# Optimization experiments

Measured on AMD Instinct MI355X. Metric: run time of the kernel, lower is better.

The kernel has to match this reference:

```python
import jax, jax.numpy as jnp
import numpy as np

TINY = 1e-15
EPS = 1e-6  # float32 eps from the torch module
C = 1.0
S = 1.0 / np.sqrt(C)
SQRTC = np.sqrt(C)


def _sinhc(z):
    # stable sinh(z)/z with small-argument Taylor branch
    y = jnp.sinh(z) / jnp.maximum(z, EPS)
    y0 = 1.0 + z * z / 6.0
    return jnp.where(jnp.abs(z) < EPS, y0, y)


def _beta(x):
    denom = jnp.sqrt(1.0 + C * jnp.sum(x * x, axis=-1, keepdims=True))
    return 1.0 / jnp.maximum(denom, TINY)


def _log0(y):
    s = jnp.linalg.norm(y, axis=-1, keepdims=True)
    coef = jnp.arcsinh(s / S) / jnp.maximum(s / S, EPS)
    return coef * y


def _exp0(v):
    r = jnp.linalg.norm(v, axis=-1, keepdims=True)
    coef = jnp.sinh(r / S) / jnp.maximum(r / S, EPS)
    return coef * v


def _proj_tan0(v, max_norm=20.0):
    r = jnp.maximum(jnp.linalg.norm(v, axis=-1, keepdims=True), EPS)
    return jnp.minimum(max_norm / r, 1.0) * v


def _pt_0_to_y(y, v):
    b = _beta(y)
    coef = C * b / (1.0 + b)
    dot = jnp.sum(y * v, axis=-1, keepdims=True)
    return v + coef * dot * y


def _gyro_add(x, y):
    b_x = _beta(x)
    b_y = _beta(y)
    s2 = S * S
    xy = jnp.sum(x * y, axis=-1, keepdims=True)
    coef = b_x / (1.0 + b_x) * (xy / s2) + (1.0 - b_y) / b_y
    return x + y + coef * x


def _exp_map(x, v):
    s2 = S * S
    x_norm2 = jnp.sum(x * x, axis=-1, keepdims=True)
    v_norm2 = jnp.sum(v * v, axis=-1, keepdims=True)
    dot_x_v = jnp.sum(x * v, axis=-1, keepdims=True)
    g_pvv = jnp.maximum(v_norm2 - dot_x_v * dot_x_v / (s2 + x_norm2), TINY)
    r_g = jnp.sqrt(g_pvv)
    b_x = _beta(x)
    coef1 = b_x / (1.0 + b_x)
    coef2 = -(C * b_x ** 3) / jnp.maximum(1.0 + b_x, TINY) ** 2
    dpi_v = coef1 * v + coef2 * dot_x_v * x
    lambda_x = (1.0 + b_x) / jnp.maximum(b_x, TINY)
    z_arg = jnp.clip(SQRTC * r_g, -20.0, 20.0)
    w = lambda_x * _sinhc(z_arg) * dpi_v
    return _gyro_add(x, w)


def setup_inputs() -> dict:
    key = jax.random.key(0)
    k1, k2, k3 = jax.random.split(key, 3)
    N, D_IN, D_OUT = 16384, 2048, 2048
    x = jax.random.normal(k1, (N, D_IN), dtype=jnp.float32)
    # weight scaled ~1/sqrt(d_in) so tangent norms stay in a sane hyperbolic range
    W = jax.random.normal(k2, (D_OUT, D_IN), dtype=jnp.float32) * (1.0 / np.sqrt(D_IN))
    b = jax.random.normal(k3, (D_OUT,), dtype=jnp.float32) * 0.01
    return {"x": x, "W": W, "b": b}


def reference(x, W, b):
    # PV fully-connected layer: log map -> linear -> exp map -> transported bias
    v = _log0(x)                 # [N, d_in] tangent at origin
    u = v @ W.T                  # [N, d_out]
    u = _proj_tan0(u)            # tangent norm clamp (max_norm=20)
    y = _exp0(u)                 # [N, d_out] PV point
    bt = _pt_0_to_y(y, b)        # parallel transport bias tangent 0 -> y
    out = _exp_map(y, bt)        # geodesic step (includes gyro_add)
    return out
```

## Files before the change

### kernel.cpp

```cpp
#include <hip/hip_runtime.h>
#include <stdint.h>

typedef __bf16 bf16_t;
typedef __bf16 bf16x8 __attribute__((ext_vector_type(8)));
typedef float floatx4 __attribute__((ext_vector_type(4)));
typedef float f32x4 __attribute__((ext_vector_type(4)));

#define N_ROWS 16384
#define D_IN   2048
#define D_OUT  2048
#define EPSF   1e-6f
#define TINYF  1e-15f

#define BM 256
#define BN 256
#define BK 32
#define NT 192

__device__ __forceinline__ void load_lds16(const void* g, void* l) {
    __builtin_amdgcn_global_load_lds(
        (const __attribute__((address_space(1))) unsigned int*)(const unsigned int*)g,
        (__attribute__((address_space(3))) unsigned int*)(unsigned int*)l,
        16, 0, 0);
}

__global__ __launch_bounds__(256) void pvfc_wsplit(
    const float* __restrict__ W, bf16_t* __restrict__ Wh, bf16_t* __restrict__ Wl)
{
    const size_t i = ((size_t)blockIdx.x * 256 + threadIdx.x) * 8;
    f32x4 a = *(const f32x4*)(W + i);
    f32x4 c = *(const f32x4*)(W + i + 4);
    float v[8] = {a.x, a.y, a.z, a.w, c.x, c.y, c.z, c.w};
    bf16x8 hv, lv;
#pragma unroll
    for (int j = 0; j < 8; ++j) {
        const bf16_t h = (bf16_t)v[j];
        hv[j] = h;
        lv[j] = (bf16_t)(v[j] - (float)h);
    }
    *(bf16x8*)(Wh + i) = hv;
    *(bf16x8*)(Wl + i) = lv;
}

__global__ __launch_bounds__(256) void pvfc_prologue(
    const float* __restrict__ x, bf16_t* __restrict__ Ap)
{
    __shared__ float red[4];
    const int row = blockIdx.x, tid = threadIdx.x;
    const int lane = tid & 63, wave = tid >> 6;

    const float* xr = x + (size_t)row * D_IN + tid * 8;
    f32x4 a = __builtin_nontemporal_load((const f32x4*)xr);
    f32x4 c = __builtin_nontemporal_load((const f32x4*)(xr + 4));
    float v[8] = {a.x, a.y, a.z, a.w, c.x, c.y, c.z, c.w};

    float s = 0.f;
#pragma unroll
    for (int i = 0; i < 8; ++i) s += v[i] * v[i];
#pragma unroll
    for (int off = 32; off > 0; off >>= 1) s += __shfl_down(s, off, 64);
    if (lane == 0) red[wave] = s;
    __syncthreads();
    const float s2  = red[0] + red[1] + red[2] + red[3];
    const float nrm = sqrtf(s2);
    const float coef = asinhf(nrm) / fmaxf(nrm, EPSF);

    bf16x8 hv, lv;
#pragma unroll
    for (int j = 0; j < 8; ++j) {
        const float vi = coef * v[j];
        const bf16_t h = (bf16_t)vi;
        hv[j] = h;
        lv[j] = (bf16_t)(vi - (float)h);
    }
    bf16_t* ar = Ap + (size_t)row * (2 * D_IN);
    *(bf16x8*)(ar + tid * 8)         = hv;
    *(bf16x8*)(ar + D_IN + tid * 8)  = lv;
}

#define BAR __builtin_amdgcn_s_barrier()
#define SCHED_FENCE __builtin_amdgcn_sched_barrier(0)
#define WAIT_LGKM0 do { asm volatile("s_waitcnt lgkmcnt(0)" ::: "memory"); \
                        __builtin_amdgcn_sched_barrier(0); } while (0)
#define WAIT_VM0   do { asm volatile("s_waitcnt vmcnt(0)" ::: "memory");   \
                        __builtin_amdgcn_sched_barrier(0); } while (0)

#define READ_A4(AF, brd, h)                                                    \
    _Pragma("unroll")                                                          \
    for (int i = 0; i < 4; ++i) {                                              \
        const int mi = (h) * 4 + i;                                            \
        AF[mi] = *(const bf16x8*)&As3[(brd) * 8192 +                           \
                    (wm * 128 + mi * 16 + m16) * 32 + ((quad ^ swk) * 8)];     \
    }
#define READ_B4(BF, brd)                                                       \
    _Pragma("unroll")                                                          \
    for (int j = 0; j < 4; ++j)                                                \
        BF[j] = *(const bf16x8*)&Bs3[(brd) * 8192 +                            \
                    (wn * 64 + j * 16 + m16) * 32 + ((quad ^ swk) * 8)];
#define MFMA_G(AF, BF, g)                                                      \
    do {                                                                       \
        __builtin_amdgcn_s_setprio(1);                                         \
        _Pragma("unroll")                                                      \
        for (int i = 0; i < 2; ++i)                                            \
            _Pragma("unroll")                                                  \
            for (int j = 0; j < 4; ++j)                                        \
                acc[(g) * 2 + i][j] = __builtin_amdgcn_mfma_f32_16x16x32_bf16( \
                    AF[(g) * 2 + i], BF[j], acc[(g) * 2 + i][j], 0, 0, 0);     \
        __builtin_amdgcn_s_setprio(0);                                         \
    } while (0)

#define BODY(AC, BC, AN, BN_, brd, bst, stT)                                   \
    do {                                                                       \
        WAIT_LGKM0;                 \
        stage_tile(stT, bst);                 \
        SCHED_FENCE;                                                           \
        READ_A4(AN, brd, 0); MFMA_G(AC, BC, 0); SCHED_FENCE;                   \
        READ_A4(AN, brd, 1); MFMA_G(AC, BC, 1); SCHED_FENCE;                   \
        READ_B4(BN_, brd);   MFMA_G(AC, BC, 2); SCHED_FENCE;                   \
        MFMA_G(AC, BC, 3);                                                     \
        WAIT_VM0;                                                              \
        BAR;                                                                   \
    } while (0)

__global__ __launch_bounds__(512, 2) void pvfc_gemm(
    const bf16_t* __restrict__ A,
    const bf16_t* __restrict__ Wh, const bf16_t* __restrict__ Wl,
    float* __restrict__ U)
{
    __shared__ __align__(16) bf16_t As3[3 * BM * BK];
    __shared__ __align__(16) bf16_t Bs3[3 * BN * BK];

    const int tid  = threadIdx.x;
    const int wave = tid >> 6, lane = tid & 63;
    const int bid  = blockIdx.x;
    const int colBase = (bid & 7) * BN;
    const int rowBase = (bid >> 3) * BM;

    const int wm = wave >> 2, wn = wave & 3;
    const int m16 = lane & 15, quad = lane >> 4;
    const int swk = (m16 >> 1) & 3;

    floatx4 acc[8][4];
    bf16x8 af0[8], af1[8], bf0[4], bf1[4];
    const floatx4 z = {0.f, 0.f, 0.f, 0.f};
#pragma unroll
    for (int i = 0; i < 8; ++i)
#pragma unroll
        for (int j = 0; j < 4; ++j) acc[i][j] = z;

    const int sRow = tid >> 2;
    const int sC   = (((tid & 3) ^ ((tid >> 3) & 3)) * 8);
    auto stage_tile = [&](int tile, int b) {
        const int tt  = tile < NT ? tile : NT - 1;
        const int seg = tt >> 6;
        const int k0  = (tt & 63) * BK;
        const size_t aOff = (size_t)((seg == 1) ? D_IN : 0) + k0;
        const bf16_t* Wp  = (seg == 2) ? Wl : Wh;
        bf16_t* da = As3 + b * 8192 + wave * 512;
        bf16_t* db = Bs3 + b * 8192 + wave * 512;
        load_lds16(A + (size_t)(rowBase + sRow) * (2 * D_IN) + aOff + sC, da);
        load_lds16(A + (size_t)(rowBase + 128 + sRow) * (2 * D_IN) + aOff + sC,
                   da + 4096);
        load_lds16(Wp + (size_t)(colBase + sRow) * D_IN + k0 + sC, db);
        load_lds16(Wp + (size_t)(colBase + 128 + sRow) * D_IN + k0 + sC,
                   db + 4096);
    };

    stage_tile(0, 0);
    stage_tile(1, 1);
    WAIT_VM0;
    BAR;
    READ_A4(af0, 0, 0); READ_A4(af0, 0, 1); READ_B4(bf0, 0);

#pragma clang loop unroll(disable)
    for (int t = 0; t < NT; t += 6) {
        BODY(af0, bf0, af1, bf1, 1, 2, t + 2);
        BODY(af1, bf1, af0, bf0, 2, 0, t + 3);
        BODY(af0, bf0, af1, bf1, 0, 1, t + 4);
        BODY(af1, bf1, af0, bf0, 1, 2, t + 5);
        BODY(af0, bf0, af1, bf1, 2, 0, t + 6);
        BODY(af1, bf1, af0, bf0, 0, 1, t + 7);
    }

#pragma unroll
    for (int mi = 0; mi < 8; ++mi)
#pragma unroll
        for (int ni = 0; ni < 4; ++ni) {
            const int col = colBase + wn * 64 + ni * 16 + m16;
            float* up = U + (size_t)(rowBase + wm * 128 + mi * 16 + quad * 4) * D_OUT
                          + col;
#pragma unroll
            for (int r = 0; r < 4; ++r)
                __builtin_nontemporal_store(acc[mi][ni][r], up + (size_t)r * D_OUT);
        }
}

__global__ __launch_bounds__(256) void pvfc_epilogue(
    const float* __restrict__ U, const float* __restrict__ bvec,
    float* __restrict__ out)
{
    __shared__ float red[12];
    const int row = blockIdx.x, tid = threadIdx.x;
    const int lane = tid & 63, wave = tid >> 6;

    const float* ur = U + (size_t)row * D_OUT + tid * 8;
    float u[8];
    { f32x4 a = __builtin_nontemporal_load((const f32x4*)ur);
      f32x4 c = __builtin_nontemporal_load((const f32x4*)(ur + 4));
      u[0]=a.x;u[1]=a.y;u[2]=a.z;u[3]=a.w;u[4]=c.x;u[5]=c.y;u[6]=c.z;u[7]=c.w; }
    float b[8];
    { const float* br = bvec + tid * 8;
      f32x4 a = *(const f32x4*)br, c = *(const f32x4*)(br + 4);
      b[0]=a.x;b[1]=a.y;b[2]=a.z;b[3]=a.w;b[4]=c.x;b[5]=c.y;b[6]=c.z;b[7]=c.w; }

    float su2 = 0.f, sub = 0.f, sbb = 0.f;
#pragma unroll
    for (int i = 0; i < 8; ++i) { su2 += u[i]*u[i]; sub += u[i]*b[i]; sbb += b[i]*b[i]; }
#pragma unroll
    for (int off = 32; off > 0; off >>= 1) {
        su2 += __shfl_down(su2, off, 64);
        sub += __shfl_down(sub, off, 64);
        sbb += __shfl_down(sbb, off, 64);
    }
    if (lane == 0) { red[wave] = su2; red[4 + wave] = sub; red[8 + wave] = sbb; }
    __syncthreads();
    su2 = red[0] + red[1] + red[2] + red[3];
    sub = red[4] + red[5] + red[6] + red[7];
    sbb = red[8] + red[9] + red[10] + red[11];

    const float r0 = sqrtf(su2);
    const float t  = fminf(20.f / fmaxf(r0, EPSF), 1.f);
    const float rp = t * r0;
    const float coef_e = sinhf(rp) / fmaxf(rp, EPSF);
    const float P  = coef_e * t;
    const float yn2 = P * P * su2;
    const float beta = 1.f / fmaxf(sqrtf(1.f + yn2), TINYF);
    const float c  = beta / (1.f + beta);
    const float d  = P * sub;
    const float vn2   = sbb + c * d * d * (2.f + c * yn2);
    const float dotxv = d * (1.f + c * yn2);
    const float g  = fmaxf(vn2 - dotxv * dotxv / (1.f + yn2), TINYF);
    const float rg = sqrtf(g);
    const float coef1 = beta / (1.f + beta);
    const float t1 = fmaxf(1.f + beta, TINYF);
    const float coef2 = -(beta * beta * beta) / (t1 * t1);
    const float lam = (1.f + beta) / fmaxf(beta, TINYF);
    const float z  = fminf(rg, 20.f);
    const float sc = (fabsf(z) < EPSF) ? (1.f + z * z * (1.f / 6.f))
                                       : (sinhf(z) / fmaxf(z, EPSF));
    const float L = lam * sc;
    const float alpha = L * coef1;
    const float gamma = L * (coef1 * c * d + coef2 * dotxv);
    const float wn2 = alpha * alpha * sbb + 2.f * alpha * gamma * d + gamma * gamma * yn2;
    const float bw  = 1.f / fmaxf(sqrtf(1.f + wn2), TINYF);
    const float xy  = alpha * d + gamma * yn2;
    const float coefg = coef1 * xy + (1.f - bw) / bw;
    const float Ascale = P * (1.f + gamma + coefg);

    float* orow = out + (size_t)row * D_OUT + tid * 8;
    f32x4 o0, o1;
    o0.x = Ascale*u[0] + alpha*b[0]; o0.y = Ascale*u[1] + alpha*b[1];
    o0.z = Ascale*u[2] + alpha*b[2]; o0.w = Ascale*u[3] + alpha*b[3];
    o1.x = Ascale*u[4] + alpha*b[4]; o1.y = Ascale*u[5] + alpha*b[5];
    o1.z = Ascale*u[6] + alpha*b[6]; o1.w = Ascale*u[7] + alpha*b[7];
    __builtin_nontemporal_store(o0, (f32x4*)orow);
    __builtin_nontemporal_store(o1, (f32x4*)(orow + 4));
}

extern "C" void kernel_launch(void* const* d_in, const int* in_sizes, int n_in,
                              void* d_out, int out_size, void* d_ws, size_t ws_size,
                              hipStream_t stream)
{
    const float* x = (const float*)d_in[0];
    const float* W = (const float*)d_in[1];
    const float* b = (const float*)d_in[2];
    float* out = (float*)d_out;

    bf16_t* Wh = (bf16_t*)d_ws;
    bf16_t* Wl = Wh + (size_t)D_OUT * D_IN;
    char*   rest = (char*)(Wl + (size_t)D_OUT * D_IN);
    const size_t wbytes = (size_t)D_OUT * D_IN * 2 * 2;
    const size_t avail  = (ws_size > wbytes) ? ws_size - wbytes : 0;
    int chunk = (int)((avail / 16384 / 256) * 256);
    if (chunk <= 0) chunk = 256;
    if (chunk > N_ROWS) chunk = N_ROWS;

    bf16_t* Ap = (bf16_t*)rest;
    float*  U  = (float*)(rest + (size_t)chunk * (2 * D_IN) * 2);

    pvfc_wsplit<<<(D_OUT * D_IN) / (256 * 8), 256, 0, stream>>>(W, Wh, Wl);
    for (int r0 = 0; r0 < N_ROWS; r0 += chunk) {
        const int rows = (N_ROWS - r0 < chunk) ? (N_ROWS - r0) : chunk;
        pvfc_prologue<<<rows, 256, 0, stream>>>(x + (size_t)r0 * D_IN, Ap);
        pvfc_gemm<<<dim3(D_OUT / BN * (rows / BM)), 512, 0, stream>>>(Ap, Wh, Wl, U);
        pvfc_epilogue<<<rows, 256, 0, stream>>>(U, b, out + (size_t)r0 * D_OUT);
    }
}
```

Measured before the change: 709.8 us.

## Fuse three split-bf16 GEMM passes into one K loop with fragment reuse

The GEMM previously ran three sequential K sweeps (Ah·Wh, Al·Wh, Ah·Wl) as 192 tiles. Now each K step stages all four operand pieces (Ah, Al, Wh, Wl) into one double-buffered LDS region and issues the three MFMA products per step. This reuses the Ah and Wh register fragments across two products each, cuts LDS reads and loop iterations, and moves from triple buffering with cross-tile register prefetch to double buffering. The cost is twice the LDS footprint per stage, which may lower occupancy below two blocks per CU, and less overlap between LDS reads and MFMAs within a step.

```diff
diff --git a/kernel.cpp b/kernel.cpp
--- a/kernel.cpp
+++ b/kernel.cpp
@@ -15,7 +15,7 @@
 #define BM 256
 #define BN 256
 #define BK 32
-#define NT 192
+#define NK 64
 
 __device__ __forceinline__ void load_lds16(const void* g, void* l) {
     __builtin_amdgcn_global_load_lds(
@@ -80,44 +80,48 @@
 
 #define BAR __builtin_amdgcn_s_barrier()
 #define SCHED_FENCE __builtin_amdgcn_sched_barrier(0)
-#define WAIT_LGKM0 do { asm volatile("s_waitcnt lgkmcnt(0)" ::: "memory"); \
-                        __builtin_amdgcn_sched_barrier(0); } while (0)
 #define WAIT_VM0   do { asm volatile("s_waitcnt vmcnt(0)" ::: "memory");   \
                         __builtin_amdgcn_sched_barrier(0); } while (0)
 
-#define READ_A4(AF, brd, h)                                                    \
+#define UOFF(bb, unit) ((bb) * 32768 + (unit) * 8192)
+
+#define RD_A8(AF, bb, u)                                                       \
     _Pragma("unroll")                                                          \
-    for (int i = 0; i < 4; ++i) {                                              \
-        const int mi = (h) * 4 + i;                                            \
-        AF[mi] = *(const bf16x8*)&As3[(brd) * 8192 +                           \
-                    (wm * 128 + mi * 16 + m16) * 32 + ((quad ^ swk) * 8)];     \
-    }
-#define READ_B4(BF, brd)                                                       \
+    for (int mi = 0; mi < 8; ++mi)                                             \
+        AF[mi] = *(const bf16x8*)&Sh[UOFF(bb, u) +                             \
+                    (wm * 128 + mi * 16 + m16) * 32 + ((quad ^ swk) * 8)];
+#define RD_B4(BF, bb, u)                                                       \
     _Pragma("unroll")                                                          \
     for (int j = 0; j < 4; ++j)                                                \
-        BF[j] = *(const bf16x8*)&Bs3[(brd) * 8192 +                            \
+        BF[j] = *(const bf16x8*)&Sh[UOFF(bb, u) +                              \
                     (wn * 64 + j * 16 + m16) * 32 + ((quad ^ swk) * 8)];
-#define MFMA_G(AF, BF, g)                                                      \
+#define MFMA_P(AF, BF)                                                         \
     do {                                                                       \
         __builtin_amdgcn_s_setprio(1);                                         \
         _Pragma("unroll")                                                      \
-        for (int i = 0; i < 2; ++i)                                            \
+        for (int i = 0; i < 8; ++i)                                            \
             _Pragma("unroll")                                                  \
             for (int j = 0; j < 4; ++j)                                        \
-                acc[(g) * 2 + i][j] = __builtin_amdgcn_mfma_f32_16x16x32_bf16( \
-                    AF[(g) * 2 + i], BF[j], acc[(g) * 2 + i][j], 0, 0, 0);     \
+                acc[i][j] = __builtin_amdgcn_mfma_f32_16x16x32_bf16(           \
+                    AF[i], BF[j], acc[i][j], 0, 0, 0);                         \
         __builtin_amdgcn_s_setprio(0);                                         \
     } while (0)
 
-#define BODY(AC, BC, AN, BN_, brd, bst, stT)                                   \
+#define BODY(bb, nb, t1)                                                       \
     do {                                                                       \
-        WAIT_LGKM0;                 \
-        stage_tile(stT, bst);                 \
-        SCHED_FENCE;                                                           \
-        READ_A4(AN, brd, 0); MFMA_G(AC, BC, 0); SCHED_FENCE;                   \
-        READ_A4(AN, brd, 1); MFMA_G(AC, BC, 1); SCHED_FENCE;                   \
-        READ_B4(BN_, brd);   MFMA_G(AC, BC, 2); SCHED_FENCE;                   \
-        MFMA_G(AC, BC, 3);                                                     \
+        stage_tile(t1, nb);                         \
+        SCHED_FENCE;                                                           \
+        RD_B4(wfh, bb, 2); RD_A8(ah, bb, 0);                                   \
+        SCHED_FENCE;                                                           \
+        MFMA_P(ah, wfh);                                            \
+        SCHED_FENCE;                                                           \
+        RD_A8(al, bb, 1);                                                      \
+        SCHED_FENCE;                                                           \
+        MFMA_P(al, wfh);                                            \
+        SCHED_FENCE;                                                           \
+        RD_B4(wfl, bb, 3);                                                     \
+        SCHED_FENCE;                                                           \
+        MFMA_P(ah, wfl);                                            \
         WAIT_VM0;                                                              \
         BAR;                                                                   \
     } while (0)
@@ -127,8 +131,7 @@
     const bf16_t* __restrict__ Wh, const bf16_t* __restrict__ Wl,
     float* __restrict__ U)
 {
-    __shared__ __align__(16) bf16_t As3[3 * BM * BK];
-    __shared__ __align__(16) bf16_t Bs3[3 * BN * BK];
+    __shared__ __align__(16) bf16_t Sh[2 * 4 * 8192];
 
     const int tid  = threadIdx.x;
     const int wave = tid >> 6, lane = tid & 63;
@@ -141,7 +144,7 @@
     const int swk = (m16 >> 1) & 3;
 
     floatx4 acc[8][4];
-    bf16x8 af0[8], af1[8], bf0[4], bf1[4];
+    bf16x8 ah[8], al[8], wfh[4], wfl[4];
     const floatx4 z = {0.f, 0.f, 0.f, 0.f};
 #pragma unroll
     for (int i = 0; i < 8; ++i)
@@ -151,35 +154,33 @@
     const int sRow = tid >> 2;
     const int sC   = (((tid & 3) ^ ((tid >> 3) & 3)) * 8);
     auto stage_tile = [&](int tile, int b) {
-        const int tt  = tile < NT ? tile : NT - 1;
-        const int seg = tt >> 6;
-        const int k0  = (tt & 63) * BK;
-        const size_t aOff = (size_t)((seg == 1) ? D_IN : 0) + k0;
-        const bf16_t* Wp  = (seg == 2) ? Wl : Wh;
-        bf16_t* da = As3 + b * 8192 + wave * 512;
-        bf16_t* db = Bs3 + b * 8192 + wave * 512;
-        load_lds16(A + (size_t)(rowBase + sRow) * (2 * D_IN) + aOff + sC, da);
-        load_lds16(A + (size_t)(rowBase + 128 + sRow) * (2 * D_IN) + aOff + sC,
-                   da + 4096);
-        load_lds16(Wp + (size_t)(colBase + sRow) * D_IN + k0 + sC, db);
-        load_lds16(Wp + (size_t)(colBase + 128 + sRow) * D_IN + k0 + sC,
-                   db + 4096);
+        const int tt = tile < NK ? tile : NK - 1;
+        const int k0 = tt * BK;
+        bf16_t* base = Sh + b * 32768 + wave * 512;
+        const bf16_t* a0 = A + (size_t)(rowBase + sRow) * (2 * D_IN) + k0 + sC;
+        const bf16_t* a1 = A + (size_t)(rowBase + 128 + sRow) * (2 * D_IN) + k0 + sC;
+        load_lds16(a0, base);
+        load_lds16(a1, base + 4096);
+        load_lds16(a0 + D_IN, base + 8192);
+        load_lds16(a1 + D_IN, base + 8192 + 4096);
+        const bf16_t* w0 = Wh + (size_t)(colBase + sRow) * D_IN + k0 + sC;
+        const bf16_t* w1 = Wh + (size_t)(colBase + 128 + sRow) * D_IN + k0 + sC;
+        load_lds16(w0, base + 16384);
+        load_lds16(w1, base + 16384 + 4096);
+        const bf16_t* v0 = Wl + (size_t)(colBase + sRow) * D_IN + k0 + sC;
+        const bf16_t* v1 = Wl + (size_t)(colBase + 128 + sRow) * D_IN + k0 + sC;
+        load_lds16(v0, base + 24576);
+        load_lds16(v1, base + 24576 + 4096);
     };
 
     stage_tile(0, 0);
-    stage_tile(1, 1);
     WAIT_VM0;
     BAR;
-    READ_A4(af0, 0, 0); READ_A4(af0, 0, 1); READ_B4(bf0, 0);
 
 #pragma clang loop unroll(disable)
-    for (int t = 0; t < NT; t += 6) {
-        BODY(af0, bf0, af1, bf1, 1, 2, t + 2);
-        BODY(af1, bf1, af0, bf0, 2, 0, t + 3);
-        BODY(af0, bf0, af1, bf1, 0, 1, t + 4);
-        BODY(af1, bf1, af0, bf0, 1, 2, t + 5);
-        BODY(af0, bf0, af1, bf1, 2, 0, t + 6);
-        BODY(af1, bf1, af0, bf0, 0, 1, t + 7);
+    for (int t = 0; t < NK; t += 2) {
+        BODY(0, 1, t + 1);
+        BODY(1, 0, t + 2);
     }
 
 #pragma unroll
```

Result: faster. 602.0 us (-15.2%).
